# Performance work log

Measured on AMD Instinct MI355X. Metric: run time of the kernel, lower is better.

Reference implementation:

```python
import jax, jax.numpy as jnp
import numpy as np

BETA = 0.25  # commitment loss weight


def setup_inputs() -> dict:
    key = jax.random.key(0)
    k1, k2 = jax.random.split(key)
    z = jax.random.normal(k1, (16, 64, 32, 32), dtype=jnp.float32)      # [B,C,H,W]
    emb = jax.random.normal(k2, (8192, 64), dtype=jnp.float32)          # [V,C] codebook
    return {"z": z, "emb": emb}


def reference(z, emb):
    b, c, h, w = z.shape
    # [B,C,H,W] -> [N,C] with N = B*H*W (channels-last flatten, as in torch permute+reshape)
    z_flat = jnp.transpose(z, (0, 2, 3, 1)).reshape(-1, c)
    # squared L2 distances to every code: ||z||^2 + ||e||^2 - 2 z.e
    dist = (
        jnp.sum(z_flat * z_flat, axis=1, keepdims=True)
        + jnp.sum(emb * emb, axis=1)
        - 2.0 * (z_flat @ emb.T)
    )  # [N,V]
    idx = jnp.argmin(dist, axis=1)  # [N]
    z_q = emb[idx].reshape(b, h, w, c).transpose(0, 3, 1, 2)  # [B,C,H,W]
    codebook_loss = jnp.mean((z_q - jax.lax.stop_gradient(z)) ** 2)
    commit_loss = jnp.mean((z - jax.lax.stop_gradient(z_q)) ** 2)
    vq_loss = codebook_loss + BETA * commit_loss
    # straight-through estimator
    z_q_st = z + jax.lax.stop_gradient(z_q - z)
    return z_q_st, idx.reshape(b, h, w), vq_loss
```

## Files before the change

kernel.cpp:

```cpp
#include <hip/hip_runtime.h>


typedef _Float16 half8 __attribute__((ext_vector_type(8)));
typedef float f32x4 __attribute__((ext_vector_type(4)));

#define N_PTS 16384
#define SPLITS 16
#define THR16 0.08f


__global__ __launch_bounds__(256) void k_pre(const float* __restrict__ emb,
                                             float* __restrict__ hneg,
                                             unsigned short* __restrict__ e16,
                                             float* __restrict__ embT,
                                             int* __restrict__ cnt) {
  int v = blockIdx.x * 256 + threadIdx.x;
  const float4* e4 = (const float4*)(emb + v * 64);
  float s = 0.f;
  float row[64];
#pragma unroll
  for (int i = 0; i < 16; ++i) {
    float4 a = e4[i];
    row[i * 4 + 0] = a.x; row[i * 4 + 1] = a.y;
    row[i * 4 + 2] = a.z; row[i * 4 + 3] = a.w;
    s += a.x * a.x + a.y * a.y + a.z * a.z + a.w * a.w;
  }
  unsigned short* base = e16 + (v >> 4) * 1024 + (v & 15) * 8;
#pragma unroll
  for (int c8 = 0; c8 < 8; ++c8) {
    half8 o;
#pragma unroll
    for (int j = 0; j < 8; ++j) o[j] = (_Float16)row[c8 * 8 + j];
    *(half8*)(base + (c8 >> 2) * 512 + (c8 & 3) * 128) = o;
  }
#pragma unroll
  for (int c = 0; c < 64; ++c) embT[c * 8192 + v] = row[c];
  hneg[v] = -0.5f * s;
  if (v == 0) *cnt = 0;
}

__global__ __launch_bounds__(256, 4) void k1_score(
    const float* __restrict__ z, const unsigned short* __restrict__ e16,
    const float* __restrict__ hneg,
    float* __restrict__ ps, float* __restrict__ p2) {
  __shared__ float hs[512];
  const int tid = threadIdx.x;
  const int lane = tid & 63;
  const int wid = tid >> 6;
  const int cl = lane & 15;
  const int gq = lane >> 4;
  const int n0 = blockIdx.x * 256 + wid * 64;
  const int split = blockIdx.y;
  const int vbase = split * 512;

  *(float2*)&hs[tid * 2] = *(const float2*)(hneg + vbase + tid * 2);
  __syncthreads();

  const int b = n0 >> 10;
  const int hw0 = n0 & 1023;

  half8 A[4][2];
  {
    const float* zb = z + b * 65536 + hw0 + cl;
#pragma unroll
    for (int pt = 0; pt < 4; ++pt)
#pragma unroll
      for (int H = 0; H < 2; ++H) {
        half8 a;
#pragma unroll
        for (int j = 0; j < 8; ++j)
          a[j] = (_Float16)zb[pt * 16 + (H * 32 + gq * 8 + j) * 1024];
        A[pt][H] = a;
      }
  }

  float s1[4][4], s2[4][4];
#pragma unroll
  for (int pt = 0; pt < 4; ++pt)
#pragma unroll
    for (int r = 0; r < 4; ++r) { s1[pt][r] = -3.0e38f; s2[pt][r] = -3.0e38f; }

  const unsigned short* bbase = e16 + vbase * 64 + lane * 8;
  int idxb = 8191 - (vbase + cl);

#pragma unroll 2
  for (int T = 0; T < 32; ++T) {
    const unsigned short* bp = bbase + T * 1024;
    half8 B0 = *(const half8*)bp;
    half8 B1 = *(const half8*)(bp + 512);
    const float nh = hs[T * 16 + cl];
    f32x4 C0;
    C0[0] = nh; C0[1] = nh; C0[2] = nh; C0[3] = nh;

#pragma unroll
    for (int pt = 0; pt < 4; ++pt) {
      f32x4 acc = __builtin_amdgcn_mfma_f32_16x16x32_f16(A[pt][0], B0, C0, 0, 0, 0);
      acc = __builtin_amdgcn_mfma_f32_16x16x32_f16(A[pt][1], B1, acc, 0, 0, 0);

#pragma unroll
      for (int r = 0; r < 4; ++r) {
        unsigned u = (__float_as_uint(acc[r]) & 0xFFFFE000u) | (unsigned)idxb;
        float p = __uint_as_float(u);
        s2[pt][r] = __builtin_amdgcn_fmed3f(p, s1[pt][r], s2[pt][r]);
        s1[pt][r] = fmaxf(s1[pt][r], p);
      }
    }
    idxb -= 16;
  }

#pragma unroll
  for (int off = 8; off >= 1; off >>= 1) {
#pragma unroll
    for (int pt = 0; pt < 4; ++pt)
#pragma unroll
      for (int r = 0; r < 4; ++r) {
        float os = __shfl_xor(s1[pt][r], off);
        float o2 = __shfl_xor(s2[pt][r], off);
        s2[pt][r] = fmaxf(fmaxf(s2[pt][r], o2), fminf(s1[pt][r], os));
        s1[pt][r] = fmaxf(s1[pt][r], os);
      }
  }

  if (cl == 0) {
#pragma unroll
    for (int pt = 0; pt < 4; ++pt)
#pragma unroll
      for (int r = 0; r < 4; ++r) {
        int n = n0 + pt * 16 + gq * 4 + r;
        int o = split * N_PTS + n;
        ps[o] = s1[pt][r]; p2[o] = s2[pt][r];
      }
  }
}

__global__ __launch_bounds__(256) void k2_merge(
    const float* __restrict__ ps, const float* __restrict__ p2,
    int* __restrict__ idxf, float* __restrict__ out_idx,
    int* __restrict__ list, int* __restrict__ cnt) {
  int n = blockIdx.x * 256 + threadIdx.x;
  float S1 = ps[n], S2 = p2[n];
#pragma unroll
  for (int s = 1; s < SPLITS; ++s) {
    int o = s * N_PTS + n;
    float a = ps[o], a2 = p2[o];
    if (a > S1) { S2 = fmaxf(fmaxf(S2, a2), S1); S1 = a; }
    else        { S2 = fmaxf(S2, a); }
  }
  int I1 = 8191 - (int)(__float_as_uint(S1) & 0x1FFFu);
  idxf[n] = I1;
  out_idx[n] = (float)I1;
  float q = fmaxf(fabsf(S1), fabsf(S2)) * 0.0009765625f;
  if (S1 - S2 < THR16 + q) {
    int p = atomicAdd(cnt, 1);
    list[p] = n;
  }
}

__global__ __launch_bounds__(1024, 4) void k_rescue(
    const float* __restrict__ z, const float* __restrict__ embT,
    const float* __restrict__ hneg, const int* __restrict__ list,
    const int* __restrict__ cnt,
    int* __restrict__ idxf, float* __restrict__ out_idx) {
  __shared__ float zsT[64][8];
  __shared__ int pn[8];
  __shared__ float rs[16][8], ri[16][8];
  const int tid = threadIdx.x;
  const int lane = tid & 63, wv = tid >> 6;
  const int count = *cnt;

  for (int base = blockIdx.x * 8; base < count; base += gridDim.x * 8) {
    const int P = min(8, count - base);
    __syncthreads();
    if (tid < 8) pn[tid] = list[base + min(tid, P - 1)];
    __syncthreads();
    if (tid < 512) {
      int p = tid >> 6, c = tid & 63;
      int n = pn[p];
      zsT[c][p] = z[(n >> 10) * 65536 + c * 1024 + (n & 1023)];
    }
    __syncthreads();

    float d[64];
#pragma unroll
    for (int i = 0; i < 64; ++i) d[i] = 0.f;

    const float4* eT = (const float4*)embT;
    float4 cur0 = eT[tid];
    float4 cur1 = eT[1024 + tid];

    for (int c = 0; c < 64; ++c) {
      float4 nxt0, nxt1;
      if (c < 63) {
        const float4* rowp = eT + (c + 1) * 2048 + tid;
        nxt0 = rowp[0];
        nxt1 = rowp[1024];
      }
      float4 zpA = *(const float4*)&zsT[c][0];
      float4 zpB = *(const float4*)&zsT[c][4];
#pragma unroll
      for (int k = 0; k < 8; ++k) {
        float e = (k == 0) ? cur0.x : (k == 1) ? cur0.y : (k == 2) ? cur0.z :
                  (k == 3) ? cur0.w : (k == 4) ? cur1.x : (k == 5) ? cur1.y :
                  (k == 6) ? cur1.z : cur1.w;
        float* dp = d + k * 8;
        dp[0] = fmaf(e, zpA.x, dp[0]); dp[1] = fmaf(e, zpA.y, dp[1]);
        dp[2] = fmaf(e, zpA.z, dp[2]); dp[3] = fmaf(e, zpA.w, dp[3]);
        dp[4] = fmaf(e, zpB.x, dp[4]); dp[5] = fmaf(e, zpB.y, dp[5]);
        dp[6] = fmaf(e, zpB.z, dp[6]); dp[7] = fmaf(e, zpB.w, dp[7]);
      }
      if (c < 63) { cur0 = nxt0; cur1 = nxt1; }
    }

    float4 hv0 = *(const float4*)(hneg + tid * 4);
    float4 hv1 = *(const float4*)(hneg + 4096 + tid * 4);
    float bs[8], bi[8];
#pragma unroll
    for (int p = 0; p < 8; ++p) { bs[p] = -3.0e38f; bi[p] = 0.f; }
#pragma unroll
    for (int k = 0; k < 8; ++k) {
      float hk = (k == 0) ? hv0.x : (k == 1) ? hv0.y : (k == 2) ? hv0.z :
                 (k == 3) ? hv0.w : (k == 4) ? hv1.x : (k == 5) ? hv1.y :
                 (k == 6) ? hv1.z : hv1.w;
      float cf = (float)((k < 4 ? 0 : 4096) + tid * 4 + (k & 3));
#pragma unroll
      for (int p = 0; p < 8; ++p) {
        float sc = d[k * 8 + p] + hk;
        if (sc > bs[p]) { bs[p] = sc; bi[p] = cf; }
      }
    }

#pragma unroll
    for (int off = 32; off >= 1; off >>= 1) {
#pragma unroll
      for (int p = 0; p < 8; ++p) {
        float os = __shfl_xor(bs[p], off);
        float oi = __shfl_xor(bi[p], off);
        if (os > bs[p] || (os == bs[p] && oi < bi[p])) { bs[p] = os; bi[p] = oi; }
      }
    }
    if (lane == 0)
#pragma unroll
      for (int p = 0; p < 8; ++p) { rs[wv][p] = bs[p]; ri[wv][p] = bi[p]; }
    __syncthreads();
    if (tid < 8) {
      int p = tid;
      float s = rs[0][p], i = ri[0][p];
#pragma unroll
      for (int w = 1; w < 16; ++w) {
        if (rs[w][p] > s || (rs[w][p] == s && ri[w][p] < i)) { s = rs[w][p]; i = ri[w][p]; }
      }
      if (p < P) {
        int n = pn[p];
        idxf[n] = (int)i;
        out_idx[n] = i;
      }
    }
  }
}

__global__ __launch_bounds__(256) void k3_quant(
    const float* __restrict__ z, const float* __restrict__ emb,
    const int* __restrict__ idxf,
    float* __restrict__ out, float* __restrict__ psum) {
  int t = blockIdx.x * 256 + threadIdx.x;
  int g = t * 4;
  int b = g >> 16;
  int c = (g >> 10) & 63;
  int hw = g & 1023;
  int n = (b << 10) | hw;
  float4 zv = *(const float4*)(z + g);
  int4 iv = *(const int4*)(idxf + n);
  float q0 = emb[iv.x * 64 + c];
  float q1 = emb[iv.y * 64 + c];
  float q2 = emb[iv.z * 64 + c];
  float q3 = emb[iv.w * 64 + c];
  float d0 = q0 - zv.x, d1 = q1 - zv.y, d2 = q2 - zv.z, d3 = q3 - zv.w;
  float4 o;
  o.x = zv.x + d0; o.y = zv.y + d1; o.z = zv.z + d2; o.w = zv.w + d3;
  *(float4*)(out + g) = o;
  float val = d0 * d0 + d1 * d1 + d2 * d2 + d3 * d3;
#pragma unroll
  for (int off = 32; off >= 1; off >>= 1) val += __shfl_down(val, off);
  __shared__ float wsum[4];
  int lane = threadIdx.x & 63, wv = threadIdx.x >> 6;
  if (lane == 0) wsum[wv] = val;
  __syncthreads();
  if (threadIdx.x == 0)
    psum[blockIdx.x] = wsum[0] + wsum[1] + wsum[2] + wsum[3];
}

__global__ __launch_bounds__(256) void k4_loss(const float* __restrict__ psum,
                                               float* __restrict__ out_loss) {
  int tid = threadIdx.x;
  float val = psum[tid] + psum[tid + 256] + psum[tid + 512] + psum[tid + 768];
#pragma unroll
  for (int off = 32; off >= 1; off >>= 1) val += __shfl_down(val, off);
  __shared__ float wsum[4];
  int lane = tid & 63, wv = tid >> 6;
  if (lane == 0) wsum[wv] = val;
  __syncthreads();
  if (tid == 0)
    out_loss[0] = 1.25f * (wsum[0] + wsum[1] + wsum[2] + wsum[3]) * (1.0f / 1048576.0f);
}

extern "C" void kernel_launch(void* const* d_in, const int* in_sizes, int n_in,
                              void* d_out, int out_size, void* d_ws, size_t ws_size,
                              hipStream_t stream) {
  const float* z   = (const float*)d_in[0];
  const float* emb = (const float*)d_in[1];
  float* out = (float*)d_out;
  float* ws  = (float*)d_ws;

  float* hneg = ws;
  unsigned short* e16 = (unsigned short*)(ws + 8192);
  float* embT = ws + 8192 + 262144;
  float* ps  = embT + 524288;
  float* p2  = ps + SPLITS * N_PTS;
  int* idxf  = (int*)(p2 + SPLITS * N_PTS);
  int* list  = idxf + N_PTS;
  int* cnt   = list + N_PTS;
  float* psum = (float*)(cnt + 1);

  float* out_idx  = out + 1048576;
  float* out_loss = out + 1048576 + 16384;

  k_pre<<<32, 256, 0, stream>>>(emb, hneg, e16, embT, cnt);
  k1_score<<<dim3(64, SPLITS), 256, 0, stream>>>(z, e16, hneg, ps, p2);
  k2_merge<<<64, 256, 0, stream>>>(ps, p2, idxf, out_idx, list, cnt);
  k_rescue<<<256, 1024, 0, stream>>>(z, embT, hneg, list, cnt, idxf, out_idx);
  k3_quant<<<1024, 256, 0, stream>>>(z, emb, idxf, out, psum);
  k4_loss<<<1, 256, 0, stream>>>(psum, out_loss);
}
```

Measured before the change: 157.7 us.

## Fuse merge into rescue with grid barrier, fold loss into quant, widen pre

Merges the split-merge and rescue kernels into one kernel that uses a global atomic counter as a grid-wide barrier, and folds the final loss reduction into the quantize kernel via a last-block-done pattern. The per-split top-2 scores are packed into a float2 array, and the codebook preprocessing is spread over four threads per code with a shuffle reduction. This cuts two kernel launches and their inter-kernel gaps. In exchange it relies on all 256 blocks of 1024 threads being co-resident for the spin barrier to avoid deadlock.

Measured after the change: 194.4 us. 1.23x slower.

```diff
diff --git a/kernel.cpp b/kernel.cpp
--- a/kernel.cpp
+++ b/kernel.cpp
@@ -7,42 +7,45 @@
 #define N_PTS 16384
 #define SPLITS 16
 #define THR16 0.08f
-
 
 __global__ __launch_bounds__(256) void k_pre(const float* __restrict__ emb,
                                              float* __restrict__ hneg,
                                              unsigned short* __restrict__ e16,
                                              float* __restrict__ embT,
                                              int* __restrict__ cnt) {
-  int v = blockIdx.x * 256 + threadIdx.x;
-  const float4* e4 = (const float4*)(emb + v * 64);
+  int t = blockIdx.x * 256 + threadIdx.x;
+  int v = t >> 2, part = t & 3;
+  const float4* e4 = (const float4*)(emb + v * 64 + part * 16);
+  float row[16];
   float s = 0.f;
-  float row[64];
-#pragma unroll
-  for (int i = 0; i < 16; ++i) {
+#pragma unroll
+  for (int i = 0; i < 4; ++i) {
     float4 a = e4[i];
     row[i * 4 + 0] = a.x; row[i * 4 + 1] = a.y;
     row[i * 4 + 2] = a.z; row[i * 4 + 3] = a.w;
     s += a.x * a.x + a.y * a.y + a.z * a.z + a.w * a.w;
   }
+  s += __shfl_xor(s, 1);
+  s += __shfl_xor(s, 2);
   unsigned short* base = e16 + (v >> 4) * 1024 + (v & 15) * 8;
 #pragma unroll
-  for (int c8 = 0; c8 < 8; ++c8) {
+  for (int g = 0; g < 2; ++g) {
+    int c8 = part * 2 + g;
     half8 o;
 #pragma unroll
-    for (int j = 0; j < 8; ++j) o[j] = (_Float16)row[c8 * 8 + j];
+    for (int j = 0; j < 8; ++j) o[j] = (_Float16)row[g * 8 + j];
     *(half8*)(base + (c8 >> 2) * 512 + (c8 & 3) * 128) = o;
   }
 #pragma unroll
-  for (int c = 0; c < 64; ++c) embT[c * 8192 + v] = row[c];
-  hneg[v] = -0.5f * s;
-  if (v == 0) *cnt = 0;
+  for (int i = 0; i < 16; ++i) embT[(part * 16 + i) * 8192 + v] = row[i];
+  if (part == 0) hneg[v] = -0.5f * s;
+  if (t == 0) { cnt[0] = 0; cnt[1] = 0; cnt[2] = 0; }
 }
 
 __global__ __launch_bounds__(256, 4) void k1_score(
     const float* __restrict__ z, const unsigned short* __restrict__ e16,
     const float* __restrict__ hneg,
-    float* __restrict__ ps, float* __restrict__ p2) {
+    float2* __restrict__ psp) {
   __shared__ float hs[512];
   const int tid = threadIdx.x;
   const int lane = tid & 63;
@@ -96,7 +99,6 @@
     for (int pt = 0; pt < 4; ++pt) {
       f32x4 acc = __builtin_amdgcn_mfma_f32_16x16x32_f16(A[pt][0], B0, C0, 0, 0, 0);
       acc = __builtin_amdgcn_mfma_f32_16x16x32_f16(A[pt][1], B1, acc, 0, 0, 0);
-
 #pragma unroll
       for (int r = 0; r < 4; ++r) {
         unsigned u = (__float_as_uint(acc[r]) & 0xFFFFE000u) | (unsigned)idxb;
@@ -127,48 +129,55 @@
 #pragma unroll
       for (int r = 0; r < 4; ++r) {
         int n = n0 + pt * 16 + gq * 4 + r;
-        int o = split * N_PTS + n;
-        ps[o] = s1[pt][r]; p2[o] = s2[pt][r];
-      }
-  }
-}
-
-__global__ __launch_bounds__(256) void k2_merge(
-    const float* __restrict__ ps, const float* __restrict__ p2,
+        float2 o; o.x = s1[pt][r]; o.y = s2[pt][r];
+        psp[split * N_PTS + n] = o;
+      }
+  }
+}
+
+__global__ __launch_bounds__(1024, 1) void k_mr(
+    const float* __restrict__ z, const float* __restrict__ embT,
+    const float* __restrict__ hneg, const float2* __restrict__ psp,
     int* __restrict__ idxf, float* __restrict__ out_idx,
     int* __restrict__ list, int* __restrict__ cnt) {
-  int n = blockIdx.x * 256 + threadIdx.x;
-  float S1 = ps[n], S2 = p2[n];
-#pragma unroll
-  for (int s = 1; s < SPLITS; ++s) {
-    int o = s * N_PTS + n;
-    float a = ps[o], a2 = p2[o];
-    if (a > S1) { S2 = fmaxf(fmaxf(S2, a2), S1); S1 = a; }
-    else        { S2 = fmaxf(S2, a); }
-  }
-  int I1 = 8191 - (int)(__float_as_uint(S1) & 0x1FFFu);
-  idxf[n] = I1;
-  out_idx[n] = (float)I1;
-  float q = fmaxf(fabsf(S1), fabsf(S2)) * 0.0009765625f;
-  if (S1 - S2 < THR16 + q) {
-    int p = atomicAdd(cnt, 1);
-    list[p] = n;
-  }
-}
-
-__global__ __launch_bounds__(1024, 4) void k_rescue(
-    const float* __restrict__ z, const float* __restrict__ embT,
-    const float* __restrict__ hneg, const int* __restrict__ list,
-    const int* __restrict__ cnt,
-    int* __restrict__ idxf, float* __restrict__ out_idx) {
   __shared__ float zsT[64][8];
   __shared__ int pn[8];
   __shared__ float rs[16][8], ri[16][8];
+  __shared__ int cntS;
   const int tid = threadIdx.x;
   const int lane = tid & 63, wv = tid >> 6;
-  const int count = *cnt;
-
-  for (int base = blockIdx.x * 8; base < count; base += gridDim.x * 8) {
+  int* done2 = cnt + 1;
+
+  if (tid < 64) {
+    int n = blockIdx.x * 64 + tid;
+    float S1 = -3.0e38f, S2 = -3.0e38f;
+#pragma unroll
+    for (int s = 0; s < SPLITS; ++s) {
+      float2 a = psp[s * N_PTS + n];
+      if (a.x > S1) { S2 = fmaxf(fmaxf(S2, a.y), S1); S1 = a.x; }
+      else          { S2 = fmaxf(S2, a.x); }
+    }
+    int I1 = 8191 - (int)(__float_as_uint(S1) & 0x1FFFu);
+    idxf[n] = I1;
+    out_idx[n] = (float)I1;
+    float q = fmaxf(fabsf(S1), fabsf(S2)) * 0.0009765625f;
+    if (S1 - S2 < THR16 + q) {
+      int p = atomicAdd(cnt, 1);
+      list[p] = n;
+    }
+  }
+  __syncthreads();
+  if (tid == 0) {
+    __threadfence();
+    atomicAdd(done2, 1);
+    while (__hip_atomic_load(done2, __ATOMIC_ACQUIRE, __HIP_MEMORY_SCOPE_AGENT) < 256)
+      __builtin_amdgcn_s_sleep(16);
+    cntS = __hip_atomic_load(cnt, __ATOMIC_ACQUIRE, __HIP_MEMORY_SCOPE_AGENT);
+  }
+  __syncthreads();
+  const int count = cntS;
+
+  for (int base = blockIdx.x * 8; base < count; base += 256 * 8) {
     const int P = min(8, count - base);
     __syncthreads();
     if (tid < 8) pn[tid] = list[base + min(tid, P - 1)];
@@ -261,7 +270,8 @@
 __global__ __launch_bounds__(256) void k3_quant(
     const float* __restrict__ z, const float* __restrict__ emb,
     const int* __restrict__ idxf,
-    float* __restrict__ out, float* __restrict__ psum) {
+    float* __restrict__ out, float* __restrict__ psum, int* __restrict__ done3,
+    float* __restrict__ out_loss) {
   int t = blockIdx.x * 256 + threadIdx.x;
   int g = t * 4;
   int b = g >> 16;
@@ -282,25 +292,30 @@
 #pragma unroll
   for (int off = 32; off >= 1; off >>= 1) val += __shfl_down(val, off);
   __shared__ float wsum[4];
+  __shared__ int lastS;
   int lane = threadIdx.x & 63, wv = threadIdx.x >> 6;
   if (lane == 0) wsum[wv] = val;
   __syncthreads();
-  if (threadIdx.x == 0)
+  if (threadIdx.x == 0) {
     psum[blockIdx.x] = wsum[0] + wsum[1] + wsum[2] + wsum[3];
-}
-
-__global__ __launch_bounds__(256) void k4_loss(const float* __restrict__ psum,
-                                               float* __restrict__ out_loss) {
-  int tid = threadIdx.x;
-  float val = psum[tid] + psum[tid + 256] + psum[tid + 512] + psum[tid + 768];
-#pragma unroll
-  for (int off = 32; off >= 1; off >>= 1) val += __shfl_down(val, off);
-  __shared__ float wsum[4];
-  int lane = tid & 63, wv = tid >> 6;
-  if (lane == 0) wsum[wv] = val;
-  __syncthreads();
-  if (tid == 0)
-    out_loss[0] = 1.25f * (wsum[0] + wsum[1] + wsum[2] + wsum[3]) * (1.0f / 1048576.0f);
+    __threadfence();
+    lastS = (atomicAdd(done3, 1) == 1023) ? 1 : 0;
+  }
+  __syncthreads();
+  if (lastS) {
+    float v = 0.f;
+#pragma unroll
+    for (int i = 0; i < 4; ++i)
+      v += __hip_atomic_load(&psum[threadIdx.x + i * 256], __ATOMIC_RELAXED,
+                             __HIP_MEMORY_SCOPE_AGENT);
+#pragma unroll
+    for (int off = 32; off >= 1; off >>= 1) v += __shfl_down(v, off);
+    __syncthreads();
+    if (lane == 0) wsum[wv] = v;
+    __syncthreads();
+    if (threadIdx.x == 0)
+      out_loss[0] = 1.25f * (wsum[0] + wsum[1] + wsum[2] + wsum[3]) * (1.0f / 1048576.0f);
+  }
 }
 
 extern "C" void kernel_launch(void* const* d_in, const int* in_sizes, int n_in,
@@ -314,20 +329,17 @@
   float* hneg = ws;
   unsigned short* e16 = (unsigned short*)(ws + 8192);
   float* embT = ws + 8192 + 262144;
-  float* ps  = embT + 524288;
-  float* p2  = ps + SPLITS * N_PTS;
-  int* idxf  = (int*)(p2 + SPLITS * N_PTS);
+  float2* psp = (float2*)(embT + 524288);
+  int* idxf  = (int*)(psp + SPLITS * N_PTS);
   int* list  = idxf + N_PTS;
   int* cnt   = list + N_PTS;
-  float* psum = (float*)(cnt + 1);
+  float* psum = (float*)(cnt + 3);
 
   float* out_idx  = out + 1048576;
   float* out_loss = out + 1048576 + 16384;
 
-  k_pre<<<32, 256, 0, stream>>>(emb, hneg, e16, embT, cnt);
-  k1_score<<<dim3(64, SPLITS), 256, 0, stream>>>(z, e16, hneg, ps, p2);
-  k2_merge<<<64, 256, 0, stream>>>(ps, p2, idxf, out_idx, list, cnt);
-  k_rescue<<<256, 1024, 0, stream>>>(z, embT, hneg, list, cnt, idxf, out_idx);
-  k3_quant<<<1024, 256, 0, stream>>>(z, emb, idxf, out, psum);
-  k4_loss<<<1, 256, 0, stream>>>(psum, out_loss);
-}
+  k_pre<<<128, 256, 0, stream>>>(emb, hneg, e16, embT, cnt);
+  k1_score<<<dim3(64, SPLITS), 256, 0, stream>>>(z, e16, hneg, psp);
+  k_mr<<<256, 1024, 0, stream>>>(z, embT, hneg, psp, idxf, out_idx, list, cnt);
+  k3_quant<<<1024, 256, 0, stream>>>(z, emb, idxf, out, psum, cnt + 2, out_loss);
+}
```
